# Optimization experiments

Measured on AMD Instinct MI355X. Metric: run time of the kernel, lower is better.

The kernel has to match this reference:

```python
import jax, jax.numpy as jnp
import numpy as np

B, N, T, OBS, ACT, M, EMB = 128, 128, 256, 512, 64, 16, 128
H = T // 2  # bi-LSTM hidden per direction
EPS = 1e-5


def _ln(x, g, b):
    mu = x.mean(-1, keepdims=True)
    var = ((x - mu) ** 2).mean(-1, keepdims=True)
    return (x - mu) / jnp.sqrt(var + EPS) * g + b


def _lstm_dir(xs, Wih, Whh, bih, bhh):
    # xs: [m, T] -> hidden states [m, H]; torch gate order i,f,g,o
    h0 = jnp.zeros(xs.shape[:-2] + (H,), xs.dtype)

    def cell(carry, x):
        h, c = carry
        z = x @ Wih.T + h @ Whh.T + bih + bhh
        i, f, g, o = jnp.split(z, 4, axis=-1)
        c = jax.nn.sigmoid(f) * c + jax.nn.sigmoid(i) * jnp.tanh(g)
        h = jax.nn.sigmoid(o) * jnp.tanh(c)
        return (h, c), h

    (_, _), hs = jax.lax.scan(cell, (h0, h0), xs)
    return hs


def setup_inputs() -> dict:
    key = jax.random.key(0)
    ks = iter(jax.random.split(key, 32))

    def lin(fi, shape):
        return jax.random.normal(next(ks), shape, jnp.float32) / float(np.sqrt(fi))

    z = lambda *s: jnp.zeros(s, jnp.float32)
    o = lambda *s: jnp.ones(s, jnp.float32)
    return dict(
        obs=jax.random.normal(next(ks), (B, N, OBS), jnp.float32),
        W1=lin(OBS, (OBS, T)), b1=z(T), g1=o(T), be1=z(T),
        W2=lin(T, (T, T)), b2=z(T), g2=o(T), be2=z(T),
        Wa1=lin(T, (T, EMB)), ba1=z(EMB),
        Wa2=lin(EMB, (EMB, EMB)), ba2=z(EMB),
        Wa3=lin(EMB, (EMB, 1)), ba3=z(1),
        Wf_ih=lin(T, (4 * H, T)), Wf_hh=lin(H, (4 * H, H)), bf_ih=z(4 * H), bf_hh=z(4 * H),
        Wb_ih=lin(T, (4 * H, T)), Wb_hh=lin(H, (4 * H, H)), bb_ih=z(4 * H), bb_hh=z(4 * H),
        W3=lin(T, (T, T)), b3=z(T), g3=o(T), be3=z(T),
        W4=lin(T, (T, ACT)), b4=z(ACT), g4=o(ACT), be4=z(ACT),
    )


def reference(obs, W1, b1, g1, be1, W2, b2, g2, be2,
              Wa1, ba1, Wa2, ba2, Wa3, ba3,
              Wf_ih, Wf_hh, bf_ih, bf_hh, Wb_ih, Wb_hh, bb_ih, bb_hh,
              W3, b3, g3, be3, W4, b4, g4, be4):
    # actor_1: Linear -> LN -> ReLU -> Linear -> LN
    h = jax.nn.relu(_ln(obs @ W1 + b1, g1, be1))
    thoughts = _ln(h @ W2 + b2, g2, be2)              # [B,N,T]

    # attention unit: 2-layer MLP + sigmoid
    a = jax.nn.relu(thoughts @ Wa1 + ba1)
    a = jax.nn.relu(a @ Wa2 + ba2)
    init_prob = jax.nn.sigmoid(a @ Wa3 + ba3)          # [B,N,1]
    is_init = init_prob[..., 0] > 0.4                  # [B,N]

    # pairwise squared distances via bmm (same expansion as torch code)
    dot = jnp.einsum('bit,bjt->bij', thoughts, thoughts)
    sq = jnp.diagonal(dot, axis1=1, axis2=2)           # [B,N]
    dists = sq[:, None, :] - 2.0 * dot + sq[:, :, None]

    # top-m nearest neighbors per agent, then agent-index order (matches j-loop order)
    _, idx = jax.lax.top_k(-dists, M)                  # [B,N,M]
    idx = jnp.sort(idx, axis=-1)

    bidx = jnp.arange(B)[:, None, None]
    aidx = jnp.arange(N)[None, :, None]
    C = jnp.zeros((B, N, N), thoughts.dtype).at[bidx, aidx, idx].set(1.0)
    C = C * is_init[..., None].astype(thoughts.dtype)

    old_thoughts = thoughts

    # sequential per-agent communication: gather group, bi-LSTM, scatter back
    def update_one(th, grp_idx, flags):
        def step(t, inp):
            gi, fl = inp
            grp = t[gi]                                 # [M,T]
            hf = _lstm_dir(grp, Wf_ih, Wf_hh, bf_ih, bf_hh)
            hb = _lstm_dir(grp[::-1], Wb_ih, Wb_hh, bb_ih, bb_hh)[::-1]
            integ = jnp.concatenate([hf, hb], -1)       # [M,T]
            t = t.at[gi].set(jnp.where(fl, integ, grp))
            return t, None
        t, _ = jax.lax.scan(step, th, (grp_idx, flags))
        return t

    new_thoughts = jax.vmap(update_one)(thoughts, idx, is_init)

    # actor_2: ReLU -> Linear -> LN -> Linear -> LN -> Tanh
    h2 = jax.nn.relu(new_thoughts)
    h2 = _ln(h2 @ W3 + b3, g3, be3)
    acts = jnp.tanh(_ln(h2 @ W4 + b4, g4, be4))
    return acts, C, init_prob, is_init, new_thoughts, old_thoughts
```

## Files before the change

### kernel.cpp

```cpp
#include <hip/hip_runtime.h>
#include <math.h>

typedef __attribute__((ext_vector_type(8))) short bf16x8;
typedef __attribute__((ext_vector_type(4))) float f32x4;

__device__ __forceinline__ unsigned short f2bf(float x) {
    unsigned int u = __float_as_uint(x);
    u += 0x7fffu + ((u >> 16) & 1u);
    return (unsigned short)(u >> 16);
}
__device__ __forceinline__ float bf2f(unsigned short b) {
    return __uint_as_float(((unsigned int)b) << 16);
}
__device__ __forceinline__ float fsig(float z) {
    float e = __expf(-z);
    return __builtin_amdgcn_rcpf(1.f + e);
}
__device__ __forceinline__ float ftanh(float x) {
    float ax = fabsf(x);
    float e = __expf(-2.f * ax);
    float r = (1.f - e) * __builtin_amdgcn_rcpf(1.f + e);
    return copysignf(r, x);
}
__device__ __forceinline__ bf16x8 pack8(float4 a, float4 b) {
    bf16x8 r;
    r[0] = (short)f2bf(a.x); r[1] = (short)f2bf(a.y);
    r[2] = (short)f2bf(a.z); r[3] = (short)f2bf(a.w);
    r[4] = (short)f2bf(b.x); r[5] = (short)f2bf(b.y);
    r[6] = (short)f2bf(b.z); r[7] = (short)f2bf(b.w);
    return r;
}

__global__ void prep_kernel(const float* __restrict__ Wf_ih, const float* __restrict__ Wb_ih,
                            const float* __restrict__ Wf_hh, const float* __restrict__ Wb_hh,
                            const float* __restrict__ bf_ih, const float* __restrict__ bf_hh,
                            const float* __restrict__ bb_ih, const float* __restrict__ bb_hh,
                            unsigned short* __restrict__ wihbf,
                            unsigned short* __restrict__ whhbf,
                            float* __restrict__ biasz) {
    int i = blockIdx.x * 256 + threadIdx.x;
    if (i < 131072) {
        wihbf[i]          = f2bf(Wf_ih[i]);
        wihbf[131072 + i] = f2bf(Wb_ih[i]);
    }
    if (i < 65536) {
        whhbf[i]         = f2bf(Wf_hh[i]);
        whhbf[65536 + i] = f2bf(Wb_hh[i]);
    }
    if (i < 512) {
        biasz[i]       = bf_ih[i] + bf_hh[i];
        biasz[512 + i] = bb_ih[i] + bb_hh[i];
    }
}

__global__ __launch_bounds__(256) void gemm64(const float* __restrict__ A,
                                              const float* __restrict__ Bm,
                                              const float* __restrict__ bias,
                                              float* __restrict__ C,
                                              int M, int N, int K, int flags) {
    __shared__ float As[16][68];
    __shared__ float Bs[16][68];
    const int t = threadIdx.x;
    const int row0 = blockIdx.y * 64, col0 = blockIdx.x * 64;
    const int tm = t >> 4, tn = t & 15;
    float acc[4][4] = {};
    for (int k0 = 0; k0 < K; k0 += 16) {
        {
            int r = t >> 2, kq = (t & 3) * 4;
            float4 v = *(const float4*)(A + (size_t)(row0 + r) * K + k0 + kq);
            if (flags & 2) {
                v.x = fmaxf(v.x, 0.f); v.y = fmaxf(v.y, 0.f);
                v.z = fmaxf(v.z, 0.f); v.w = fmaxf(v.w, 0.f);
            }
            As[kq + 0][r] = v.x; As[kq + 1][r] = v.y;
            As[kq + 2][r] = v.z; As[kq + 3][r] = v.w;
        }
        {
            int kk = t >> 4, nq = (t & 15) * 4;
            float4 v = *(const float4*)(Bm + (size_t)(k0 + kk) * N + col0 + nq);
            *(float4*)&Bs[kk][nq] = v;
        }
        __syncthreads();
#pragma unroll
        for (int kk = 0; kk < 16; ++kk) {
            float a[4], b[4];
#pragma unroll
            for (int i = 0; i < 4; ++i) a[i] = As[kk][tm * 4 + i];
#pragma unroll
            for (int j = 0; j < 4; ++j) b[j] = Bs[kk][tn * 4 + j];
#pragma unroll
            for (int i = 0; i < 4; ++i)
#pragma unroll
                for (int j = 0; j < 4; ++j) acc[i][j] = fmaf(a[i], b[j], acc[i][j]);
        }
        __syncthreads();
    }
#pragma unroll
    for (int i = 0; i < 4; ++i) {
#pragma unroll
        for (int j = 0; j < 4; ++j) {
            int col = col0 + tn * 4 + j;
            float v = acc[i][j] + (bias ? bias[col] : 0.f);
            if (flags & 1) v = fmaxf(v, 0.f);
            C[(size_t)(row0 + tm * 4 + i) * N + col] = v;
        }
    }
}

__global__ __launch_bounds__(256) void ln256_kernel(const float* __restrict__ X,
                                                    float* __restrict__ Y,
                                                    float* __restrict__ Y2,
                                                    const float* __restrict__ gam,
                                                    const float* __restrict__ bet,
                                                    int relu) {
#pragma clang fp contract(off)
    int row = blockIdx.x * 4 + (threadIdx.x >> 6);
    int l = threadIdx.x & 63;
    float4 x = *(const float4*)(X + (size_t)row * 256 + l * 4);
    float s = x.x + x.y + x.z + x.w;
#pragma unroll
    for (int d = 1; d < 64; d <<= 1) s += __shfl_xor(s, d);
    float mu = s * (1.f / 256.f);
    float d0 = x.x - mu, d1 = x.y - mu, d2 = x.z - mu, d3 = x.w - mu;
    float ss = d0 * d0 + d1 * d1 + d2 * d2 + d3 * d3;
#pragma unroll
    for (int d = 1; d < 64; d <<= 1) ss += __shfl_xor(ss, d);
    float var = ss * (1.f / 256.f);
    float sd = sqrtf(var + 1e-5f);
    float4 y;
    y.x = (d0 / sd) * gam[l * 4 + 0] + bet[l * 4 + 0];
    y.y = (d1 / sd) * gam[l * 4 + 1] + bet[l * 4 + 1];
    y.z = (d2 / sd) * gam[l * 4 + 2] + bet[l * 4 + 2];
    y.w = (d3 / sd) * gam[l * 4 + 3] + bet[l * 4 + 3];
    if (relu) {
        y.x = fmaxf(y.x, 0.f); y.y = fmaxf(y.y, 0.f);
        y.z = fmaxf(y.z, 0.f); y.w = fmaxf(y.w, 0.f);
    }
    *(float4*)(Y + (size_t)row * 256 + l * 4) = y;
    if (Y2) *(float4*)(Y2 + (size_t)row * 256 + l * 4) = y;
}

__global__ __launch_bounds__(256) void ln64_tanh_kernel(const float* __restrict__ X,
                                                        float* __restrict__ Y,
                                                        const float* __restrict__ gam,
                                                        const float* __restrict__ bet) {
#pragma clang fp contract(off)
    int row = blockIdx.x * 4 + (threadIdx.x >> 6);
    int l = threadIdx.x & 63;
    float x = X[(size_t)row * 64 + l];
    float s = x;
#pragma unroll
    for (int d = 1; d < 64; d <<= 1) s += __shfl_xor(s, d);
    float mu = s * (1.f / 64.f);
    float dx = x - mu;
    float ss = dx * dx;
#pragma unroll
    for (int d = 1; d < 64; d <<= 1) ss += __shfl_xor(ss, d);
    float var = ss * (1.f / 64.f);
    float sd = sqrtf(var + 1e-5f);
    float y = tanhf((dx / sd) * gam[l] + bet[l]);
    Y[(size_t)row * 64 + l] = y;
}

__global__ __launch_bounds__(256) void attn_head_kernel(const float* __restrict__ a2,
                                                        const float* __restrict__ Wa3,
                                                        const float* __restrict__ ba3,
                                                        float* __restrict__ outP,
                                                        float* __restrict__ outInit,
                                                        int* __restrict__ flags) {
#pragma clang fp contract(off)
    int row = blockIdx.x * 4 + (threadIdx.x >> 6);
    int l = threadIdx.x & 63;
    float s = a2[(size_t)row * 128 + l] * Wa3[l] + a2[(size_t)row * 128 + 64 + l] * Wa3[64 + l];
#pragma unroll
    for (int d = 1; d < 64; d <<= 1) s += __shfl_xor(s, d);
    s += ba3[0];
    float p = 1.f / (1.f + expf(-s));
    if (l == 0) {
        outP[row] = p;
        int f = (p > 0.4f) ? 1 : 0;
        outInit[row] = f ? 1.f : 0.f;
        flags[row] = f;
    }
}

__global__ __launch_bounds__(256) void dot_kernel(const float* __restrict__ th,
                                                  float* __restrict__ dotm) {
    __shared__ float As[16][68];
    __shared__ float Bs[16][132];
    const int b = blockIdx.x >> 1, half = blockIdx.x & 1;
    const int t = threadIdx.x;
    const int tm = t >> 4, tn = t & 15;
    float acc[4][8] = {};
    const float* base = th + (size_t)b * 128 * 256;
    for (int k0 = 0; k0 < 256; k0 += 16) {
        {
            int r = t >> 2, kq = (t & 3) * 4;
            float4 v = *(const float4*)(base + (size_t)(half * 64 + r) * 256 + k0 + kq);
            As[kq + 0][r] = v.x; As[kq + 1][r] = v.y;
            As[kq + 2][r] = v.z; As[kq + 3][r] = v.w;
        }
        {
            int n = t >> 1, kq = (t & 1) * 8;
            const float* src = base + (size_t)n * 256 + k0 + kq;
            float4 v0 = *(const float4*)src;
            float4 v1 = *(const float4*)(src + 4);
            Bs[kq + 0][n] = v0.x; Bs[kq + 1][n] = v0.y;
            Bs[kq + 2][n] = v0.z; Bs[kq + 3][n] = v0.w;
            Bs[kq + 4][n] = v1.x; Bs[kq + 5][n] = v1.y;
            Bs[kq + 6][n] = v1.z; Bs[kq + 7][n] = v1.w;
        }
        __syncthreads();
#pragma unroll
        for (int kk = 0; kk < 16; ++kk) {
            float a[4], bb[8];
#pragma unroll
            for (int i = 0; i < 4; ++i) a[i] = As[kk][tm * 4 + i];
#pragma unroll
            for (int j = 0; j < 8; ++j) bb[j] = Bs[kk][tn * 8 + j];
#pragma unroll
            for (int i = 0; i < 4; ++i)
#pragma unroll
                for (int j = 0; j < 8; ++j) acc[i][j] = fmaf(a[i], bb[j], acc[i][j]);
        }
        __syncthreads();
    }
#pragma unroll
    for (int i = 0; i < 4; ++i)
#pragma unroll
        for (int j = 0; j < 8; ++j)
            dotm[(size_t)b * 16384 + (size_t)(half * 64 + tm * 4 + i) * 128 + tn * 8 + j] = acc[i][j];
}

__global__ void sq_kernel(const float* __restrict__ dotm, float* __restrict__ sq) {
    int i = blockIdx.x * 256 + threadIdx.x;
    int b = i >> 7, n = i & 127;
    sq[i] = dotm[(size_t)b * 16384 + (size_t)n * 129];
}

__global__ __launch_bounds__(256) void topk_kernel(const float* __restrict__ dotm,
                                                   const float* __restrict__ sq,
                                                   const int* __restrict__ flags,
                                                   float* __restrict__ outC,
                                                   int* __restrict__ idxb) {
#pragma clang fp contract(off)
    int row = blockIdx.x * 4 + (threadIdx.x >> 6);
    int l = threadIdx.x & 63;
    int b = row >> 7;
    const float* drow = dotm + (size_t)row * 128;
    float sqi = sq[row];
    float t0 = 2.f * drow[l];
    float v0 = sq[b * 128 + l] - t0; v0 = v0 + sqi;
    float t1 = 2.f * drow[64 + l];
    float v1 = sq[b * 128 + 64 + l] - t1; v1 = v1 + sqi;

    unsigned long long mlo = 0ull, mhi = 0ull;
#pragma unroll 1
    for (int n = 0; n < 16; ++n) {
        float bv = v0; int bi = l;
        if (v1 < bv) { bv = v1; bi = 64 + l; }
#pragma unroll
        for (int d = 1; d < 64; d <<= 1) {
            float ov = __shfl_xor(bv, d);
            int oi = __shfl_xor(bi, d);
            if (ov < bv || (ov == bv && oi < bi)) { bv = ov; bi = oi; }
        }
        if (bi < 64) mlo |= (1ull << bi); else mhi |= (1ull << (bi - 64));
        if (l == bi) v0 = __builtin_inff();
        if (64 + l == bi) v1 = __builtin_inff();
    }
    float fl = (flags[row] != 0) ? 1.f : 0.f;
    outC[(size_t)row * 128 + l]      = fl * (((mlo >> l) & 1ull) ? 1.f : 0.f);
    outC[(size_t)row * 128 + 64 + l] = fl * (((mhi >> l) & 1ull) ? 1.f : 0.f);
    if (l < 16) {
        int cnt = 0, found = -1;
        for (int jj = 0; jj < 128; ++jj) {
            bool bit = (jj < 64) ? ((mlo >> jj) & 1ull) : ((mhi >> (jj - 64)) & 1ull);
            if (bit) { if (cnt == l) { found = jj; break; } ++cnt; }
        }
        idxb[(size_t)row * 16 + l] = found;
    }
}

__global__ __launch_bounds__(1024, 4) void chain_kernel(float* __restrict__ th,
                                                        const unsigned short* __restrict__ whhbf,
                                                        const unsigned short* __restrict__ wihbf,
                                                        const float* __restrict__ biasz,
                                                        const int* __restrict__ idxb,
                                                        const int* __restrict__ flags) {
    const int b = blockIdx.x;
    const int t = threadIdx.x;
    const int l = t & 63, lr = l & 15, lg = l >> 4;
    const int w = t >> 6, dir = w >> 3, wd = w & 7;

    __shared__ __align__(16) unsigned short thl[128 * 256];
    __shared__ __align__(16) unsigned short xgs[2 * 16 * 520];
    __shared__ __align__(16) unsigned short hbufs[2][2][128];
    __shared__ int idxl[128 * 16];
    __shared__ int flg[128];

    {
        int r = t >> 3, c0 = (t & 7) * 32;
        const float* src = th + (size_t)(b * 128 + r) * 256 + c0;
        char* rowb = (char*)thl + r * 512;
        int swz = (r & 7) << 4;
#pragma unroll
        for (int i = 0; i < 4; ++i) {
            float4 v0 = *(const float4*)(src + i * 8);
            float4 v1 = *(const float4*)(src + i * 8 + 4);
            *(bf16x8*)(rowb + (((c0 + i * 8) * 2) ^ swz)) = pack8(v0, v1);
        }
    }
    if (t < 128) flg[t] = flags[b * 128 + t];
    idxl[t] = idxb[(size_t)b * 2048 + t];
    idxl[t + 1024] = idxb[(size_t)b * 2048 + 1024 + t];

    bf16x8 wf[4][4];
    {
        const unsigned short* whh = whhbf + (size_t)dir * 65536;
#pragma unroll
        for (int G = 0; G < 4; ++G) {
            int gate = G * 128 + wd * 16 + lr;
#pragma unroll
            for (int kc = 0; kc < 4; ++kc)
                wf[G][kc] = *(const bf16x8*)(whh + (size_t)gate * 128 + kc * 32 + lg * 8);
        }
    }
    const unsigned short* wih = wihbf + (size_t)dir * 131072;
    float bzr[4];
#pragma unroll
    for (int ct = 0; ct < 4; ++ct) bzr[ct] = biasz[dir * 512 + wd * 64 + ct * 16 + lr];
    __syncthreads();

    for (int ag = 0; ag < 128; ++ag) {
        if (!flg[ag]) continue;
        const int* gi = &idxl[ag * 16];
        const int myrow = gi[lr];
        const int myswz = (myrow & 7) << 4;
        const char* arow = (const char*)thl + myrow * 512;

        if (t < 512) ((unsigned short*)hbufs)[t] = 0;

        {
            f32x4 xa[4];
#pragma unroll
            for (int ct = 0; ct < 4; ++ct) xa[ct] = (f32x4){0.f, 0.f, 0.f, 0.f};
#pragma unroll
            for (int kc = 0; kc < 8; ++kc) {
                bf16x8 af = *(const bf16x8*)(arow + ((kc * 64 + lg * 16) ^ myswz));
#pragma unroll
                for (int ct = 0; ct < 4; ++ct) {
                    const unsigned short* wb =
                        wih + (size_t)(wd * 64 + ct * 16 + lr) * 256 + kc * 32 + lg * 8;
                    xa[ct] = __builtin_amdgcn_mfma_f32_16x16x32_bf16(
                        af, *(const bf16x8*)wb, xa[ct], 0, 0, 0);
                }
            }
#pragma unroll
            for (int ct = 0; ct < 4; ++ct) {
                int g = wd * 64 + ct * 16 + lr;
#pragma unroll
                for (int r = 0; r < 4; ++r) {
                    int m = lg * 4 + r;
                    xgs[(dir * 16 + m) * 520 + g] = f2bf(xa[ct][r] + bzr[ct]);
                }
            }
        }
        __syncthreads();

        float xgv[4];
        {
            int m0 = dir ? 15 : 0;
            const unsigned short* xm = &xgs[(dir * 16 + m0) * 520 + wd * 16 + lr];
#pragma unroll
            for (int G = 0; G < 4; ++G) xgv[G] = bf2f(xm[G * 128]);
        }

        float cst = 0.f;
#pragma unroll 2
        for (int s = 0; s < 16; ++s) {
            const int m = dir ? (15 - s) : s;
            const int p = s & 1;
            f32x4 acc[4];
#pragma unroll
            for (int G = 0; G < 4; ++G) acc[G] = (f32x4){0.f, 0.f, 0.f, 0.f};
#pragma unroll
            for (int kc = 0; kc < 4; ++kc) {
                bf16x8 ha = *(const bf16x8*)(&hbufs[p][dir][kc * 32 + lg * 8]);
#pragma unroll
                for (int G = 0; G < 4; ++G)
                    acc[G] = __builtin_amdgcn_mfma_f32_16x16x32_bf16(ha, wf[G][kc], acc[G], 0, 0, 0);
            }
            float zi = acc[0][0] + xgv[0];
            float zf = acc[1][0] + xgv[1];
            float zg = acc[2][0] + xgv[2];
            float zo = acc[3][0] + xgv[3];
            float ig = fsig(zi), fg = fsig(zf), gv = ftanh(zg), og = fsig(zo);
            cst = fg * cst + ig * gv;
            float h = og * ftanh(cst);
            int rowm = gi[m];
            if (lg == 0) {
                int j = wd * 16 + lr;
                hbufs[p ^ 1][dir][j] = f2bf(h);
                int col = dir * 128 + j;
                *(unsigned short*)((char*)thl + rowm * 512 + ((col * 2) ^ ((rowm & 7) << 4))) =
                    f2bf(h);
            }
            if (s < 15) {
                int mn = dir ? (14 - s) : (s + 1);
                const unsigned short* xm = &xgs[(dir * 16 + mn) * 520 + wd * 16 + lr];
#pragma unroll
                for (int G = 0; G < 4; ++G) xgv[G] = bf2f(xm[G * 128]);
            }
            __syncthreads();
        }
    }

    __syncthreads();
    {
        int r = t >> 3, c0 = (t & 7) * 32;
        const char* rowb = (const char*)thl + r * 512;
        int swz = (r & 7) << 4;
        float* dst = th + (size_t)(b * 128 + r) * 256 + c0;
#pragma unroll
        for (int i = 0; i < 4; ++i) {
            bf16x8 sv = *(const bf16x8*)(rowb + (((c0 + i * 8) * 2) ^ swz));
            float4 v0, v1;
            v0.x = bf2f((unsigned short)sv[0]); v0.y = bf2f((unsigned short)sv[1]);
            v0.z = bf2f((unsigned short)sv[2]); v0.w = bf2f((unsigned short)sv[3]);
            v1.x = bf2f((unsigned short)sv[4]); v1.y = bf2f((unsigned short)sv[5]);
            v1.z = bf2f((unsigned short)sv[6]); v1.w = bf2f((unsigned short)sv[7]);
            *(float4*)(dst + i * 8) = v0;
            *(float4*)(dst + i * 8 + 4) = v1;
        }
    }
}

extern "C" void kernel_launch(void* const* d_in, const int* in_sizes, int n_in,
                              void* d_out, int out_size, void* d_ws, size_t ws_size,
                              hipStream_t stream) {
    const float* obs  = (const float*)d_in[0];
    const float* W1   = (const float*)d_in[1];
    const float* b1   = (const float*)d_in[2];
    const float* gg1  = (const float*)d_in[3];
    const float* be1  = (const float*)d_in[4];
    const float* W2   = (const float*)d_in[5];
    const float* b2   = (const float*)d_in[6];
    const float* gg2  = (const float*)d_in[7];
    const float* be2  = (const float*)d_in[8];
    const float* Wa1  = (const float*)d_in[9];
    const float* ba1  = (const float*)d_in[10];
    const float* Wa2  = (const float*)d_in[11];
    const float* ba2  = (const float*)d_in[12];
    const float* Wa3  = (const float*)d_in[13];
    const float* ba3  = (const float*)d_in[14];
    const float* Wf_ih = (const float*)d_in[15];
    const float* Wf_hh = (const float*)d_in[16];
    const float* bf_ih = (const float*)d_in[17];
    const float* bf_hh = (const float*)d_in[18];
    const float* Wb_ih = (const float*)d_in[19];
    const float* Wb_hh = (const float*)d_in[20];
    const float* bb_ih = (const float*)d_in[21];
    const float* bb_hh = (const float*)d_in[22];
    const float* W3   = (const float*)d_in[23];
    const float* b3   = (const float*)d_in[24];
    const float* gg3  = (const float*)d_in[25];
    const float* be3  = (const float*)d_in[26];
    const float* W4   = (const float*)d_in[27];
    const float* b4   = (const float*)d_in[28];
    const float* gg4  = (const float*)d_in[29];
    const float* be4  = (const float*)d_in[30];

    float* out     = (float*)d_out;
    float* out_acts = out;
    float* out_C    = out + 1048576;
    float* out_ip   = out + 3145728;
    float* out_ii   = out + 3162112;
    float* out_nt   = out + 3178496;
    float* out_ot   = out + 7372800;

    float* ws    = (float*)d_ws;
    float* h1    = ws;
    float* abuf  = ws + 4194304;
    float* a2buf = ws + 6291456;
    unsigned short* wihbf = (unsigned short*)(ws + 8388608);
    float* biasz = ws + 8519680;
    unsigned short* whhbf = (unsigned short*)(ws + 8520704);
    float* sqb   = ws + 8586240;
    int* idxb    = (int*)(ws + 8602624);
    int* flagsb  = (int*)(ws + 8864768);

    prep_kernel<<<512, 256, 0, stream>>>(Wf_ih, Wb_ih, Wf_hh, Wb_hh,
                                         bf_ih, bf_hh, bb_ih, bb_hh,
                                         wihbf, whhbf, biasz);

    gemm64<<<dim3(4, 256), 256, 0, stream>>>(obs, W1, b1, h1, 16384, 256, 512, 0);
    ln256_kernel<<<4096, 256, 0, stream>>>(h1, h1, nullptr, gg1, be1, 1);
    gemm64<<<dim3(4, 256), 256, 0, stream>>>(h1, W2, b2, out_nt, 16384, 256, 256, 0);
    ln256_kernel<<<4096, 256, 0, stream>>>(out_nt, out_nt, out_ot, gg2, be2, 0);

    gemm64<<<dim3(2, 256), 256, 0, stream>>>(out_nt, Wa1, ba1, abuf, 16384, 128, 256, 1);
    gemm64<<<dim3(2, 256), 256, 0, stream>>>(abuf, Wa2, ba2, a2buf, 16384, 128, 128, 1);
    attn_head_kernel<<<4096, 256, 0, stream>>>(a2buf, Wa3, ba3, out_ip, out_ii, flagsb);

    dot_kernel<<<256, 256, 0, stream>>>(out_nt, abuf);
    sq_kernel<<<64, 256, 0, stream>>>(abuf, sqb);
    topk_kernel<<<4096, 256, 0, stream>>>(abuf, sqb, flagsb, out_C, idxb);

    chain_kernel<<<128, 1024, 0, stream>>>(out_nt, whhbf, wihbf, biasz, idxb, flagsb);

    gemm64<<<dim3(4, 256), 256, 0, stream>>>(out_nt, W3, b3, h1, 16384, 256, 256, 2);
    ln256_kernel<<<4096, 256, 0, stream>>>(h1, h1, nullptr, gg3, be3, 0);
    gemm64<<<dim3(1, 256), 256, 0, stream>>>(h1, W4, b4, a2buf, 16384, 64, 256, 0);
    ln64_tanh_kernel<<<4096, 256, 0, stream>>>(a2buf, out_acts, gg4, be4);
}
```

Measured before the change: 3.967 ms.

## Halve chain kernel block to 512 threads with two hidden units per lane

The sequential bi-LSTM chain kernel now runs 8 waves per block instead of 16. Each wave computes two 16-wide hidden-unit slices, so each step issues 8 MFMAs and handles 8 gate values. Input-gate preactivations are packed into a per-lane bf16x8 layout so one vector load fetches all gates for a step. Hidden outputs are staged in a snapshot buffer and written back to the thought rows once per agent rather than every step. The aim is cheaper per-step barriers and shared-memory traffic, at the cost of more register pressure and longer per-wave work in the serial recurrence.

```diff
diff --git a/kernel.cpp b/kernel.cpp
--- a/kernel.cpp
+++ b/kernel.cpp
@@ -282,148 +282,160 @@
     }
 }
 
-__global__ __launch_bounds__(1024, 4) void chain_kernel(float* __restrict__ th,
-                                                        const unsigned short* __restrict__ whhbf,
-                                                        const unsigned short* __restrict__ wihbf,
-                                                        const float* __restrict__ biasz,
-                                                        const int* __restrict__ idxb,
-                                                        const int* __restrict__ flags) {
+__global__ __launch_bounds__(512, 2) void chain_kernel(float* __restrict__ th,
+                                                       const unsigned short* __restrict__ whhbf,
+                                                       const unsigned short* __restrict__ wihbf,
+                                                       const float* __restrict__ biasz,
+                                                       const int* __restrict__ idxb,
+                                                       const int* __restrict__ flags) {
     const int b = blockIdx.x;
     const int t = threadIdx.x;
     const int l = t & 63, lr = l & 15, lg = l >> 4;
-    const int w = t >> 6, dir = w >> 3, wd = w & 7;
+    const int w = t >> 6, dir = w >> 2, wd = w & 3;
 
     __shared__ __align__(16) unsigned short thl[128 * 256];
-    __shared__ __align__(16) unsigned short xgs[2 * 16 * 520];
+    __shared__ __align__(16) unsigned short xgs2[2 * 4 * 16 * 16 * 8];
+    __shared__ __align__(16) unsigned short hsnap[2][16][128];
     __shared__ __align__(16) unsigned short hbufs[2][2][128];
-    __shared__ int idxl[128 * 16];
+    __shared__ int idxl[2048];
     __shared__ int flg[128];
 
     {
-        int r = t >> 3, c0 = (t & 7) * 32;
+        int r = t >> 2, c0 = (t & 3) * 64;
         const float* src = th + (size_t)(b * 128 + r) * 256 + c0;
         char* rowb = (char*)thl + r * 512;
         int swz = (r & 7) << 4;
 #pragma unroll
-        for (int i = 0; i < 4; ++i) {
+        for (int i = 0; i < 8; ++i) {
             float4 v0 = *(const float4*)(src + i * 8);
             float4 v1 = *(const float4*)(src + i * 8 + 4);
             *(bf16x8*)(rowb + (((c0 + i * 8) * 2) ^ swz)) = pack8(v0, v1);
         }
     }
     if (t < 128) flg[t] = flags[b * 128 + t];
-    idxl[t] = idxb[(size_t)b * 2048 + t];
-    idxl[t + 1024] = idxb[(size_t)b * 2048 + 1024 + t];
-
-    bf16x8 wf[4][4];
+#pragma unroll
+    for (int c = 0; c < 4; ++c) idxl[t + c * 512] = idxb[(size_t)b * 2048 + c * 512 + t];
+
+    bf16x8 wf[4][2][4];
     {
         const unsigned short* whh = whhbf + (size_t)dir * 65536;
 #pragma unroll
-        for (int G = 0; G < 4; ++G) {
-            int gate = G * 128 + wd * 16 + lr;
-#pragma unroll
-            for (int kc = 0; kc < 4; ++kc)
-                wf[G][kc] = *(const bf16x8*)(whh + (size_t)gate * 128 + kc * 32 + lg * 8);
-        }
+        for (int G = 0; G < 4; ++G)
+#pragma unroll
+            for (int hf = 0; hf < 2; ++hf) {
+                int gate = G * 128 + wd * 32 + hf * 16 + lr;
+#pragma unroll
+                for (int kc = 0; kc < 4; ++kc)
+                    wf[G][hf][kc] = *(const bf16x8*)(whh + (size_t)gate * 128 + kc * 32 + lg * 8);
+            }
     }
     const unsigned short* wih = wihbf + (size_t)dir * 131072;
-    float bzr[4];
-#pragma unroll
-    for (int ct = 0; ct < 4; ++ct) bzr[ct] = biasz[dir * 512 + wd * 64 + ct * 16 + lr];
+    float bzr[8];
+#pragma unroll
+    for (int tt = 0; tt < 8; ++tt)
+        bzr[tt] = biasz[dir * 512 + (tt >> 1) * 128 + wd * 32 + (tt & 1) * 16 + lr];
     __syncthreads();
 
     for (int ag = 0; ag < 128; ++ag) {
         if (!flg[ag]) continue;
-        const int* gi = &idxl[ag * 16];
-        const int myrow = gi[lr];
-        const int myswz = (myrow & 7) << 4;
-        const char* arow = (const char*)thl + myrow * 512;
-
-        if (t < 512) ((unsigned short*)hbufs)[t] = 0;
+        const int gi_lr = idxl[ag * 16 + lr];
+        const int xgbase = ((dir * 4 + wd) * 16) * 16 * 8;
+
+        ((unsigned short*)hbufs)[t] = 0;
 
         {
-            f32x4 xa[4];
-#pragma unroll
-            for (int ct = 0; ct < 4; ++ct) xa[ct] = (f32x4){0.f, 0.f, 0.f, 0.f};
+            f32x4 xa[8];
+#pragma unroll
+            for (int tt = 0; tt < 8; ++tt) xa[tt] = (f32x4){0.f, 0.f, 0.f, 0.f};
+            const char* arow = (const char*)thl + gi_lr * 512;
+            const int aswz = (gi_lr & 7) << 4;
 #pragma unroll
             for (int kc = 0; kc < 8; ++kc) {
-                bf16x8 af = *(const bf16x8*)(arow + ((kc * 64 + lg * 16) ^ myswz));
-#pragma unroll
-                for (int ct = 0; ct < 4; ++ct) {
+                bf16x8 af = *(const bf16x8*)(arow + ((kc * 64 + lg * 16) ^ aswz));
+#pragma unroll
+                for (int tt = 0; tt < 8; ++tt) {
                     const unsigned short* wb =
-                        wih + (size_t)(wd * 64 + ct * 16 + lr) * 256 + kc * 32 + lg * 8;
-                    xa[ct] = __builtin_amdgcn_mfma_f32_16x16x32_bf16(
-                        af, *(const bf16x8*)wb, xa[ct], 0, 0, 0);
+                        wih + (size_t)((tt >> 1) * 128 + wd * 32 + (tt & 1) * 16 + lr) * 256 +
+                        kc * 32 + lg * 8;
+                    xa[tt] = __builtin_amdgcn_mfma_f32_16x16x32_bf16(
+                        af, *(const bf16x8*)wb, xa[tt], 0, 0, 0);
                 }
             }
 #pragma unroll
-            for (int ct = 0; ct < 4; ++ct) {
-                int g = wd * 64 + ct * 16 + lr;
-#pragma unroll
-                for (int r = 0; r < 4; ++r) {
-                    int m = lg * 4 + r;
-                    xgs[(dir * 16 + m) * 520 + g] = f2bf(xa[ct][r] + bzr[ct]);
-                }
+            for (int r = 0; r < 4; ++r) {
+                bf16x8 pk;
+#pragma unroll
+                for (int tt = 0; tt < 8; ++tt) pk[tt] = (short)f2bf(xa[tt][r] + bzr[tt]);
+                int m = lg * 4 + r;
+                *(bf16x8*)&xgs2[xgbase + (m * 16 + lr) * 8] = pk;
             }
         }
         __syncthreads();
 
-        float xgv[4];
-        {
-            int m0 = dir ? 15 : 0;
-            const unsigned short* xm = &xgs[(dir * 16 + m0) * 520 + wd * 16 + lr];
-#pragma unroll
-            for (int G = 0; G < 4; ++G) xgv[G] = bf2f(xm[G * 128]);
-        }
-
-        float cst = 0.f;
+        float cst0 = 0.f, cst1 = 0.f;
 #pragma unroll 2
         for (int s = 0; s < 16; ++s) {
             const int m = dir ? (15 - s) : s;
             const int p = s & 1;
-            f32x4 acc[4];
-#pragma unroll
-            for (int G = 0; G < 4; ++G) acc[G] = (f32x4){0.f, 0.f, 0.f, 0.f};
+            f32x4 acc[4][2];
+#pragma unroll
+            for (int G = 0; G < 4; ++G) {
+                acc[G][0] = (f32x4){0.f, 0.f, 0.f, 0.f};
+                acc[G][1] = (f32x4){0.f, 0.f, 0.f, 0.f};
+            }
 #pragma unroll
             for (int kc = 0; kc < 4; ++kc) {
                 bf16x8 ha = *(const bf16x8*)(&hbufs[p][dir][kc * 32 + lg * 8]);
 #pragma unroll
-                for (int G = 0; G < 4; ++G)
-                    acc[G] = __builtin_amdgcn_mfma_f32_16x16x32_bf16(ha, wf[G][kc], acc[G], 0, 0, 0);
-            }
-            float zi = acc[0][0] + xgv[0];
-            float zf = acc[1][0] + xgv[1];
-            float zg = acc[2][0] + xgv[2];
-            float zo = acc[3][0] + xgv[3];
-            float ig = fsig(zi), fg = fsig(zf), gv = ftanh(zg), og = fsig(zo);
-            cst = fg * cst + ig * gv;
-            float h = og * ftanh(cst);
-            int rowm = gi[m];
+                for (int G = 0; G < 4; ++G) {
+                    acc[G][0] = __builtin_amdgcn_mfma_f32_16x16x32_bf16(
+                        ha, wf[G][0][kc], acc[G][0], 0, 0, 0);
+                    acc[G][1] = __builtin_amdgcn_mfma_f32_16x16x32_bf16(
+                        ha, wf[G][1][kc], acc[G][1], 0, 0, 0);
+                }
+            }
+            bf16x8 xp = *(const bf16x8*)&xgs2[xgbase + (m * 16 + lr) * 8];
+            float zi0 = acc[0][0][0] + bf2f((unsigned short)xp[0]);
+            float zf0 = acc[1][0][0] + bf2f((unsigned short)xp[2]);
+            float zg0 = acc[2][0][0] + bf2f((unsigned short)xp[4]);
+            float zo0 = acc[3][0][0] + bf2f((unsigned short)xp[6]);
+            float zi1 = acc[0][1][0] + bf2f((unsigned short)xp[1]);
+            float zf1 = acc[1][1][0] + bf2f((unsigned short)xp[3]);
+            float zg1 = acc[2][1][0] + bf2f((unsigned short)xp[5]);
+            float zo1 = acc[3][1][0] + bf2f((unsigned short)xp[7]);
+            float i0 = fsig(zi0), f0 = fsig(zf0), g0 = ftanh(zg0), o0 = fsig(zo0);
+            cst0 = f0 * cst0 + i0 * g0;
+            float h0 = o0 * ftanh(cst0);
+            float i1 = fsig(zi1), f1 = fsig(zf1), g1 = ftanh(zg1), o1 = fsig(zo1);
+            cst1 = f1 * cst1 + i1 * g1;
+            float h1 = o1 * ftanh(cst1);
             if (lg == 0) {
-                int j = wd * 16 + lr;
-                hbufs[p ^ 1][dir][j] = f2bf(h);
-                int col = dir * 128 + j;
-                *(unsigned short*)((char*)thl + rowm * 512 + ((col * 2) ^ ((rowm & 7) << 4))) =
-                    f2bf(h);
-            }
-            if (s < 15) {
-                int mn = dir ? (14 - s) : (s + 1);
-                const unsigned short* xm = &xgs[(dir * 16 + mn) * 520 + wd * 16 + lr];
-#pragma unroll
-                for (int G = 0; G < 4; ++G) xgv[G] = bf2f(xm[G * 128]);
+                int j0 = wd * 32 + lr;
+                unsigned short hb0 = f2bf(h0), hb1 = f2bf(h1);
+                hbufs[p ^ 1][dir][j0]      = hb0;
+                hbufs[p ^ 1][dir][j0 + 16] = hb1;
+                hsnap[dir][m][j0]      = hb0;
+                hsnap[dir][m][j0 + 16] = hb1;
             }
             __syncthreads();
         }
-    }
-
-    __syncthreads();
+
+        {
+            int d2 = t >> 8, m = (t >> 4) & 15, c8 = (t & 15) * 8;
+            bf16x8 v = *(const bf16x8*)&hsnap[d2][m][c8];
+            int row = idxl[ag * 16 + m];
+            *(bf16x8*)((char*)thl + row * 512 + (((d2 * 128 + c8) * 2) ^ ((row & 7) << 4))) = v;
+        }
+        __syncthreads();
+    }
+
     {
-        int r = t >> 3, c0 = (t & 7) * 32;
+        int r = t >> 2, c0 = (t & 3) * 64;
         const char* rowb = (const char*)thl + r * 512;
         int swz = (r & 7) << 4;
         float* dst = th + (size_t)(b * 128 + r) * 256 + c0;
 #pragma unroll
-        for (int i = 0; i < 4; ++i) {
+        for (int i = 0; i < 8; ++i) {
             bf16x8 sv = *(const bf16x8*)(rowb + (((c0 + i * 8) * 2) ^ swz));
             float4 v0, v1;
             v0.x = bf2f((unsigned short)sv[0]); v0.y = bf2f((unsigned short)sv[1]);
@@ -507,7 +519,7 @@
     sq_kernel<<<64, 256, 0, stream>>>(abuf, sqb);
     topk_kernel<<<4096, 256, 0, stream>>>(abuf, sqb, flagsb, out_C, idxb);
 
-    chain_kernel<<<128, 1024, 0, stream>>>(out_nt, whhbf, wihbf, biasz, idxb, flagsb);
+    chain_kernel<<<128, 512, 0, stream>>>(out_nt, whhbf, wihbf, biasz, idxb, flagsb);
 
     gemm64<<<dim3(4, 256), 256, 0, stream>>>(out_nt, W3, b3, h1, 16384, 256, 256, 2);
     ln256_kernel<<<4096, 256, 0, stream>>>(h1, h1, nullptr, gg3, be3, 0);
```

Result: faster. 3.730 ms (-6.0%).
